# Kernel tuning notes

Measured on AMD Instinct MI355X. Metric: run time of the kernel, lower is better.

Reference implementation:

```python
import jax, jax.numpy as jnp
import numpy as np

I, H, B, T = 512, 512, 64, 1024


def _xavier(key, shape):
    fan_in, fan_out = shape
    lim = float(np.sqrt(6.0 / (fan_in + fan_out)))
    return jax.random.uniform(key, shape, jnp.float32, -lim, lim)


def setup_inputs() -> dict:
    key = jax.random.key(0)
    ks = jax.random.split(key, 9)
    inp = {"x": jax.random.normal(ks[0], (B, T, I), jnp.float32)}
    names = ["W_ii", "W_hi", "W_if", "W_hf", "W_ig", "W_hg", "W_io", "W_ho"]
    for n, k in zip(names, ks[1:]):
        shape = (I, H) if n[2] == "i" else (H, H)
        inp[n] = _xavier(k, shape)
    for n in ["b_ii", "b_hi", "b_if", "b_hf", "b_ig", "b_hg", "b_io", "b_ho"]:
        inp[n] = jnp.zeros((H,), jnp.float32)
    return inp


def _lstm(x, W_ii, b_ii, W_hi, b_hi, W_if, b_if, W_hf, b_hf,
          W_ig, b_ig, W_hg, b_hg, W_io, b_io, W_ho, b_ho):
    Bx, Tx = x.shape[0], x.shape[1]
    Hh = W_hi.shape[0]
    # Fuse the 4 input-side gate GEMMs into one: (B,T,I) @ (I,4H)
    Wx = jnp.concatenate([W_if, W_ii, W_ig, W_io], axis=1)          # (I,4H)
    bx = jnp.concatenate([b_if + b_hf, b_ii + b_hi, b_ig + b_hg, b_io + b_ho])
    Wh = jnp.concatenate([W_hf, W_hi, W_hg, W_ho], axis=1)          # (H,4H)
    x_proj = jnp.einsum("bti,ig->btg", x, Wx) + bx                  # (B,T,4H)

    def step(carry, xp_t):
        h, c = carry
        g = xp_t + h @ Wh                                           # (B,4H)
        f = jax.nn.sigmoid(g[:, 0 * Hh:1 * Hh])
        i = jax.nn.sigmoid(g[:, 1 * Hh:2 * Hh])
        gg = jnp.tanh(g[:, 2 * Hh:3 * Hh])
        o = jax.nn.sigmoid(g[:, 3 * Hh:4 * Hh])
        c = f * c + i * gg
        h = o * jnp.tanh(c)
        return (h, c), None

    h0 = jnp.zeros((Bx, Hh), x.dtype)
    c0 = jnp.zeros((Bx, Hh), x.dtype)
    (h, c), _ = jax.lax.scan(step, (h0, c0), jnp.swapaxes(x_proj, 0, 1))
    return h, c


def reference(x, W_ii, W_hi, W_if, W_hf, W_ig, W_hg, W_io, W_ho,
              b_ii, b_hi, b_if, b_hf, b_ig, b_hg, b_io, b_ho):
    return _lstm(x, W_ii, b_ii, W_hi, b_hi, W_if, b_if, W_hf, b_hf,
                 W_ig, b_ig, W_hg, b_hg, W_io, b_io, W_ho, b_ho)
```

## Files before the change

kernel.cpp:

```cpp
#include <hip/hip_runtime.h>
#include <hip/hip_bf16.h>
#include <stdint.h>

typedef __attribute__((ext_vector_type(8))) short short8;
typedef __attribute__((ext_vector_type(4))) float f32x4;
typedef __attribute__((ext_vector_type(4))) unsigned int u32x4;
typedef __attribute__((ext_vector_type(2))) unsigned int u32x2;

__device__ __forceinline__ unsigned short f2bf(float x) {
  unsigned int u = __builtin_bit_cast(unsigned int, x);
  u += 0x7FFFu + ((u >> 16) & 1u);
  return (unsigned short)(u >> 16);
}
__device__ __forceinline__ float bf2f(unsigned short u) {
  unsigned int v = ((unsigned int)u) << 16;
  return __builtin_bit_cast(float, v);
}
__device__ __forceinline__ unsigned int pk2(float a, float b) {
  return (unsigned int)f2bf(a) | ((unsigned int)f2bf(b) << 16);
}
__device__ __forceinline__ float sigm(float x) {
  return __builtin_amdgcn_rcpf(1.0f + __builtin_amdgcn_exp2f(-1.44269504f * x));
}
__device__ __forceinline__ float tanh_(float x) {
  return 2.0f * __builtin_amdgcn_rcpf(1.0f + __builtin_amdgcn_exp2f(-2.88539008f * x)) - 1.0f;
}
__device__ __forceinline__ f32x4 mfma16(short8 a, short8 b, f32x4 c) {
  return __builtin_amdgcn_mfma_f32_16x16x32_bf16(a, b, c, 0, 0, 0);
}
__device__ __forceinline__ short8 bc(u32x4 v) { return __builtin_bit_cast(short8, v); }

__global__ void lstm_prep(
    const float* __restrict__ Wif, const float* __restrict__ Wii,
    const float* __restrict__ Wig, const float* __restrict__ Wio,
    const float* __restrict__ Whf, const float* __restrict__ Whi,
    const float* __restrict__ Whg, const float* __restrict__ Who,
    const float* __restrict__ bif, const float* __restrict__ bhf,
    const float* __restrict__ bii, const float* __restrict__ bhi,
    const float* __restrict__ big, const float* __restrict__ bhg,
    const float* __restrict__ bio, const float* __restrict__ bho,
    unsigned short* __restrict__ WxT, unsigned short* __restrict__ WhT,
    float* __restrict__ bias, unsigned short* __restrict__ hring)
{
  const long NWX = 2048L * 512, NWH = 32L * 64 * 512;
  const long NR = 4L * 4 * 16 * 512;
  long total = NWX + NWH + 2048 + NR;
  for (long i = (long)blockIdx.x * blockDim.x + threadIdx.x; i < total;
       i += (long)gridDim.x * blockDim.x) {
    if (i < NWX) {
      int n = (int)(i >> 9), k = (int)(i & 511);
      int g = n >> 9, hc = n & 511;
      const float* W = (g == 0) ? Wif : (g == 1) ? Wii : (g == 2) ? Wig : Wio;
      WxT[i] = f2bf(W[k * 512 + hc]);
    } else if (i < NWX + NWH) {
      long r = i - NWX;
      int wg = (int)(r >> 15); int rest = (int)(r & 32767);
      int j = rest >> 9, k = rest & 511;
      int g = j >> 4, hc = wg * 16 + (j & 15);
      const float* W = (g == 0) ? Whf : (g == 1) ? Whi : (g == 2) ? Whg : Who;
      WhT[r] = f2bf(W[k * 512 + hc]);
    } else if (i < NWX + NWH + 2048) {
      int n = (int)(i - NWX - NWH);
      int g = n >> 9, hc = n & 511;
      const float* bi = (g == 0) ? bif : (g == 1) ? bii : (g == 2) ? big : bio;
      const float* bh = (g == 0) ? bhf : (g == 1) ? bhi : (g == 2) ? bhg : bho;
      bias[n] = bi[hc] + bh[hc];
    } else {
      long r = i - NWX - NWH - 2048;
      long rr = r & 32767;
      hring[r] = (rr < 8192) ? (unsigned short)0 : (unsigned short)0x8000u;
    }
  }
}

#define GP 56

__global__ __launch_bounds__(256) void lstm_xproj(
    const float* __restrict__ x, const unsigned short* __restrict__ WxT,
    const float* __restrict__ bias, unsigned short* __restrict__ xp)
{
  __shared__ unsigned short As[128 * GP];
  __shared__ unsigned short Bs[128 * GP];
  int bid = blockIdx.x;
  int mt = bid & 511, nt = bid >> 9;
  int m0 = mt << 7, n0 = nt << 7;
  int tid = threadIdx.x, lane = tid & 63, w = tid >> 6;
  int wm = w >> 1, wn = w & 1;
  int l15 = lane & 15, hi4 = lane >> 4;

  f32x4 acc[4][4] = {};
  int srow = tid >> 1, skq = (tid & 1) << 4;
  const float* xa = x + (size_t)(m0 + srow) * 512 + skq;
  const unsigned short* bsrc = WxT + (size_t)(n0 + srow) * 512 + skq;
  unsigned short* adst = As + srow * GP + skq;
  unsigned short* bdst = Bs + srow * GP + skq;

  for (int kt = 0; kt < 16; ++kt) {
    f32x4 a0 = *(const f32x4*)(xa + kt * 32);
    f32x4 a1 = *(const f32x4*)(xa + kt * 32 + 4);
    f32x4 a2 = *(const f32x4*)(xa + kt * 32 + 8);
    f32x4 a3 = *(const f32x4*)(xa + kt * 32 + 12);
    u32x4 wv0 = *(const u32x4*)(bsrc + kt * 32);
    u32x4 wv1 = *(const u32x4*)(bsrc + kt * 32 + 8);
    u32x4 p0, p1;
    p0[0] = pk2(a0[0], a0[1]); p0[1] = pk2(a0[2], a0[3]);
    p0[2] = pk2(a1[0], a1[1]); p0[3] = pk2(a1[2], a1[3]);
    p1[0] = pk2(a2[0], a2[1]); p1[1] = pk2(a2[2], a2[3]);
    p1[2] = pk2(a3[0], a3[1]); p1[3] = pk2(a3[2], a3[3]);
    *(u32x4*)adst = p0;  *(u32x4*)(adst + 8) = p1;
    *(u32x4*)bdst = wv0; *(u32x4*)(bdst + 8) = wv1;
    __syncthreads();
    short8 af[4], bfr[4];
    #pragma unroll
    for (int mb = 0; mb < 4; ++mb)
      af[mb] = *(const short8*)(As + (wm * 64 + mb * 16 + l15) * GP + hi4 * 8);
    #pragma unroll
    for (int nb = 0; nb < 4; ++nb)
      bfr[nb] = *(const short8*)(Bs + (wn * 64 + nb * 16 + l15) * GP + hi4 * 8);
    #pragma unroll
    for (int mb = 0; mb < 4; ++mb)
      #pragma unroll
      for (int nb = 0; nb < 4; ++nb)
        acc[mb][nb] = mfma16(af[mb], bfr[nb], acc[mb][nb]);
    __syncthreads();
  }
  #pragma unroll
  for (int nb = 0; nb < 4; ++nb) {
    int n = n0 + wn * 64 + nb * 16 + l15;
    int gate = n >> 9, hc = n & 511, wgc = hc >> 4, lcol = hc & 15;
    float bv = bias[n];
    #pragma unroll
    for (int mb = 0; mb < 4; ++mb) {
      int mbase = m0 + wm * 64 + mb * 16 + hi4 * 4;
      #pragma unroll
      for (int i = 0; i < 4; ++i) {
        int m = mbase + i;
        int tt = m & 1023, bb = m >> 10;
        int ddc = bb >> 4, rloc = bb & 15;
        int chi = rloc >> 2, cii = rloc & 3;
        size_t dst = ((((size_t)tt * 128 + ddc * 32 + wgc) * 4 + gate) * 64 +
                      (size_t)(chi * 16 + lcol)) * 4 + cii;
        xp[dst] = f2bf(acc[mb][nb][i] + bv);
      }
    }
  }
}

#define AWAIT(N) do { \
  asm volatile("s_waitcnt vmcnt(" #N ")" ::: "memory"); \
  __builtin_amdgcn_sched_barrier(0); } while (0)

#define PLD1(dst, vof, sb) \
  asm volatile("global_load_dwordx4 %0, %1, %2 sc0 sc1" \
               : "=v"(dst) : "v"(vof), "s"(sb))

#define XLD2(dst, a64) \
  asm volatile("global_load_dwordx2 %0, %1, off" : "=v"(dst) : "v"(a64))

__global__ __launch_bounds__(256, 1) void lstm_rec(
    const unsigned short* __restrict__ xp, const unsigned short* __restrict__ WhT,
    unsigned short* __restrict__ hring, float* __restrict__ out)
{
  __shared__ unsigned short hA[8192];
  __shared__ float pre[4][16][17];

  int wgG = blockIdx.x;
  int dd = wgG >> 5, wgl = wgG & 31;
  int tid = threadIdx.x, lane = tid & 63, g = tid >> 6;
  int l15 = lane & 15, hi4 = lane >> 4;

  short8 bw[16];
  {
    const unsigned short* wsrc =
        WhT + ((size_t)wgl * 64 + g * 16 + l15) * 512 + hi4 * 8;
    #pragma unroll
    for (int kk = 0; kk < 16; ++kk)
      bw[kk] = *(const short8*)(wsrc + kk * 32);
  }

  unsigned int voff[4], lbyt[4];
  #pragma unroll
  for (int k = 0; k < 4; ++k) {
    int gid = k * 256 + tid;
    int byt = gid * 16;
    int row = gid >> 6;
    voff[k] = (unsigned)byt;
    lbyt[k] = (unsigned)(byt ^ ((row & 7) << 4));
  }
  int gcol = tid & 63;
  unsigned own = (gcol == wgl * 2 || gcol == wgl * 2 + 1) ? 0xFu : 0x0u;

  const int r = (tid & 127) >> 3;
  const int cq = (tid & 7) * 2;
  float cst[2] = {0.f, 0.f};
  unsigned int vpub = (unsigned)(r * 1024 + (wgl * 16 + cq) * 2);
  unsigned int lown = (unsigned)((r * 1024 + (wgl * 16 + cq) * 2)
                                 ^ ((r & 7) << 4));

  unsigned long long xaddr = (unsigned long long)(uintptr_t)(
      xp + ((size_t)(wgG * 4 + g) * 64 + lane) * 4);

  u32x2 pc, pn;
  XLD2(pc, xaddr);

  const size_t dbase = (size_t)dd * 32768;

  u32x4 gb[4];
  {
    const unsigned short* hb = hring + dbase;
    #pragma unroll
    for (int k = 0; k < 4; ++k) PLD1(gb[k], voff[k], hb);
  }

  for (int t = 0; t < 1024; ++t) {
    const unsigned short* hb = hring + dbase + ((size_t)(t & 3) << 13);
    if (t >= 2 && tid < 128) {
      const unsigned short* hp = hring + dbase + ((size_t)((t - 2) & 3) << 13);
      unsigned int pv = 0x80008000u;
      asm volatile("global_store_dword %0, %1, %2 sc0 sc1"
                   :: "v"(vpub), "v"(pv), "s"(hp) : "memory");
    }
    {
      unsigned m = (t == 0) ? 0xFu : (0xFu & ~own);
      int spins = 0;
      for (;;) {
        AWAIT(0);
        unsigned nm = 0;
        #pragma unroll
        for (int k = 0; k < 4; ++k) {
          if ((m >> k) & 1u) {
            u32x4 v = gb[k];
            bool clean = (v[0] != 0x80008000u) && (v[1] != 0x80008000u) &&
                         (v[2] != 0x80008000u) && (v[3] != 0x80008000u);
            if (clean)
              *(u32x4*)((char*)hA + lbyt[k]) = v;
            else
              nm |= (1u << k);
          }
        }
        m = nm;
        if (m == 0u) break;
        if (++spins > (1 << 15)) break;
        #pragma unroll
        for (int k = 0; k < 4; ++k)
          if ((m >> k) & 1u) PLD1(gb[k], voff[k], hb);
      }
    }
    __syncthreads();

    f32x4 acc;
    #pragma unroll
    for (int i = 0; i < 4; ++i) {
      unsigned int dw = pc[i >> 1];
      unsigned short us = (i & 1) ? (unsigned short)(dw >> 16)
                                  : (unsigned short)(dw & 0xFFFFu);
      acc[i] = bf2f(us);
    }
    if (t < 1023) xaddr += 262144ULL;
    XLD2(pn, xaddr);

    #pragma unroll
    for (int kk = 0; kk < 16; ++kk) {
      int b0 = (l15 * 1024 + kk * 64 + hi4 * 16) ^ ((l15 & 7) << 4);
      short8 a0 = *(const short8*)((const char*)hA + b0);
      acc = mfma16(a0, bw[kk], acc);
    }
    #pragma unroll
    for (int i = 0; i < 4; ++i)
      pre[g][hi4 * 4 + i][l15] = acc[i];
    __syncthreads();

    if (t < 1023) {
      const unsigned short* hbn =
          hring + dbase + ((size_t)((t + 1) & 3) << 13);
      #pragma unroll
      for (int k = 0; k < 4; ++k)
        if (!((own >> k) & 1u)) PLD1(gb[k], voff[k], hbn);
    }

    if (tid < 128) {
      float hv[2];
      #pragma unroll
      for (int i = 0; i < 2; ++i) {
        float fg = sigm(pre[0][r][cq + i]);
        float ig = sigm(pre[1][r][cq + i]);
        float gg = tanh_(pre[2][r][cq + i]);
        float og = sigm(pre[3][r][cq + i]);
        float c = fg * cst[i] + ig * gg;
        cst[i] = c;
        hv[i] = og * tanh_(c);
      }
      if (t < 1023) {
        unsigned int u0 = f2bf(hv[0]), u1 = f2bf(hv[1]);
        if (u0 == 0x8000u) u0 = 0;
        if (u1 == 0x8000u) u1 = 0;
        unsigned int pk = u0 | (u1 << 16);
        const unsigned short* hbn =
            hring + dbase + ((size_t)((t + 1) & 3) << 13);
        asm volatile("global_store_dword %0, %1, %2 sc0 sc1"
                     :: "v"(vpub), "v"(pk), "s"(hbn) : "memory");
        *(unsigned int*)((char*)hA + lown) = pk;
      } else {
        int b = dd * 16 + r, col = wgl * 16 + cq;
        out[(size_t)b * 512 + col] = hv[0];
        out[(size_t)b * 512 + col + 1] = hv[1];
        out[32768 + (size_t)b * 512 + col] = cst[0];
        out[32768 + (size_t)b * 512 + col + 1] = cst[1];
      }
    }
    pc = pn;
  }
}

extern "C" void kernel_launch(void* const* d_in, const int* in_sizes, int n_in,
                              void* d_out, int out_size, void* d_ws, size_t ws_size,
                              hipStream_t stream) {
  const float* x   = (const float*)d_in[0];
  const float* Wii = (const float*)d_in[1];
  const float* Whi = (const float*)d_in[2];
  const float* Wif = (const float*)d_in[3];
  const float* Whf = (const float*)d_in[4];
  const float* Wig = (const float*)d_in[5];
  const float* Whg = (const float*)d_in[6];
  const float* Wio = (const float*)d_in[7];
  const float* Who = (const float*)d_in[8];
  const float* bii = (const float*)d_in[9];
  const float* bhi = (const float*)d_in[10];
  const float* bif = (const float*)d_in[11];
  const float* bhf = (const float*)d_in[12];
  const float* big = (const float*)d_in[13];
  const float* bhg = (const float*)d_in[14];
  const float* bio = (const float*)d_in[15];
  const float* bho = (const float*)d_in[16];

  char* ws = (char*)d_ws;
  size_t off = 0;
  auto alloc = [&](size_t bytes) {
    size_t p = off; off = (off + bytes + 255) & ~(size_t)255; return p;
  };
  unsigned short* WxT  = (unsigned short*)(ws + alloc(2048UL * 512 * 2));
  unsigned short* WhT  = (unsigned short*)(ws + alloc(32UL * 64 * 512 * 2));
  float*          bias = (float*)        (ws + alloc(2048UL * 4));
  unsigned short* hring= (unsigned short*)(ws + alloc(4UL * 4 * 16 * 512 * 2));
  unsigned short* xpb  = (unsigned short*)(ws + alloc(1024UL * 64 * 2048 * 2));
  if (off > ws_size) return;

  lstm_prep<<<2048, 256, 0, stream>>>(Wif, Wii, Wig, Wio, Whf, Whi, Whg, Who,
                                      bif, bhf, bii, bhi, big, bhg, bio, bho,
                                      WxT, WhT, bias, hring);
  lstm_xproj<<<8192, 256, 0, stream>>>(x, WxT, bias, xpb);
  lstm_rec<<<128, 256, 0, stream>>>(xpb, WhT, hring, (float*)d_out);
}
```

Measured before the change: 2.653 ms.

## Fuse input projection into recurrent kernel, overlapping it with the h-exchange wait

Removes the separate xproj GEMM kernel and its large bf16 intermediate buffer. Each recurrent workgroup now keeps its slice of Wx in registers and computes the x-projection for each timestep with MFMAs inside the time loop, starting from the bias. That work runs while the workgroup waits for the other workgroups to publish h. The cost is 16 more short8 registers per thread and redundant fp32 x loads from global memory on the serial critical path, since each of the 4 waves in a workgroup reads the same x rows.

```diff
diff --git a/kernel.cpp b/kernel.cpp
--- a/kernel.cpp
+++ b/kernel.cpp
@@ -5,16 +5,11 @@
 typedef __attribute__((ext_vector_type(8))) short short8;
 typedef __attribute__((ext_vector_type(4))) float f32x4;
 typedef __attribute__((ext_vector_type(4))) unsigned int u32x4;
-typedef __attribute__((ext_vector_type(2))) unsigned int u32x2;
 
 __device__ __forceinline__ unsigned short f2bf(float x) {
   unsigned int u = __builtin_bit_cast(unsigned int, x);
   u += 0x7FFFu + ((u >> 16) & 1u);
   return (unsigned short)(u >> 16);
-}
-__device__ __forceinline__ float bf2f(unsigned short u) {
-  unsigned int v = ((unsigned int)u) << 16;
-  return __builtin_bit_cast(float, v);
 }
 __device__ __forceinline__ unsigned int pk2(float a, float b) {
   return (unsigned int)f2bf(a) | ((unsigned int)f2bf(b) << 16);
@@ -73,79 +68,6 @@
   }
 }
 
-#define GP 56
-
-__global__ __launch_bounds__(256) void lstm_xproj(
-    const float* __restrict__ x, const unsigned short* __restrict__ WxT,
-    const float* __restrict__ bias, unsigned short* __restrict__ xp)
-{
-  __shared__ unsigned short As[128 * GP];
-  __shared__ unsigned short Bs[128 * GP];
-  int bid = blockIdx.x;
-  int mt = bid & 511, nt = bid >> 9;
-  int m0 = mt << 7, n0 = nt << 7;
-  int tid = threadIdx.x, lane = tid & 63, w = tid >> 6;
-  int wm = w >> 1, wn = w & 1;
-  int l15 = lane & 15, hi4 = lane >> 4;
-
-  f32x4 acc[4][4] = {};
-  int srow = tid >> 1, skq = (tid & 1) << 4;
-  const float* xa = x + (size_t)(m0 + srow) * 512 + skq;
-  const unsigned short* bsrc = WxT + (size_t)(n0 + srow) * 512 + skq;
-  unsigned short* adst = As + srow * GP + skq;
-  unsigned short* bdst = Bs + srow * GP + skq;
-
-  for (int kt = 0; kt < 16; ++kt) {
-    f32x4 a0 = *(const f32x4*)(xa + kt * 32);
-    f32x4 a1 = *(const f32x4*)(xa + kt * 32 + 4);
-    f32x4 a2 = *(const f32x4*)(xa + kt * 32 + 8);
-    f32x4 a3 = *(const f32x4*)(xa + kt * 32 + 12);
-    u32x4 wv0 = *(const u32x4*)(bsrc + kt * 32);
-    u32x4 wv1 = *(const u32x4*)(bsrc + kt * 32 + 8);
-    u32x4 p0, p1;
-    p0[0] = pk2(a0[0], a0[1]); p0[1] = pk2(a0[2], a0[3]);
-    p0[2] = pk2(a1[0], a1[1]); p0[3] = pk2(a1[2], a1[3]);
-    p1[0] = pk2(a2[0], a2[1]); p1[1] = pk2(a2[2], a2[3]);
-    p1[2] = pk2(a3[0], a3[1]); p1[3] = pk2(a3[2], a3[3]);
-    *(u32x4*)adst = p0;  *(u32x4*)(adst + 8) = p1;
-    *(u32x4*)bdst = wv0; *(u32x4*)(bdst + 8) = wv1;
-    __syncthreads();
-    short8 af[4], bfr[4];
-    #pragma unroll
-    for (int mb = 0; mb < 4; ++mb)
-      af[mb] = *(const short8*)(As + (wm * 64 + mb * 16 + l15) * GP + hi4 * 8);
-    #pragma unroll
-    for (int nb = 0; nb < 4; ++nb)
-      bfr[nb] = *(const short8*)(Bs + (wn * 64 + nb * 16 + l15) * GP + hi4 * 8);
-    #pragma unroll
-    for (int mb = 0; mb < 4; ++mb)
-      #pragma unroll
-      for (int nb = 0; nb < 4; ++nb)
-        acc[mb][nb] = mfma16(af[mb], bfr[nb], acc[mb][nb]);
-    __syncthreads();
-  }
-  #pragma unroll
-  for (int nb = 0; nb < 4; ++nb) {
-    int n = n0 + wn * 64 + nb * 16 + l15;
-    int gate = n >> 9, hc = n & 511, wgc = hc >> 4, lcol = hc & 15;
-    float bv = bias[n];
-    #pragma unroll
-    for (int mb = 0; mb < 4; ++mb) {
-      int mbase = m0 + wm * 64 + mb * 16 + hi4 * 4;
-      #pragma unroll
-      for (int i = 0; i < 4; ++i) {
-        int m = mbase + i;
-        int tt = m & 1023, bb = m >> 10;
-        int ddc = bb >> 4, rloc = bb & 15;
-        int chi = rloc >> 2, cii = rloc & 3;
-        size_t dst = ((((size_t)tt * 128 + ddc * 32 + wgc) * 4 + gate) * 64 +
-                      (size_t)(chi * 16 + lcol)) * 4 + cii;
-        xp[dst] = f2bf(acc[mb][nb][i] + bv);
-      }
-    }
-  }
-}
-
 #define AWAIT(N) do { \
   asm volatile("s_waitcnt vmcnt(" #N ")" ::: "memory"); \
   __builtin_amdgcn_sched_barrier(0); } while (0)
@@ -154,11 +76,9 @@
   asm volatile("global_load_dwordx4 %0, %1, %2 sc0 sc1" \
                : "=v"(dst) : "v"(vof), "s"(sb))
 
-#define XLD2(dst, a64) \
-  asm volatile("global_load_dwordx2 %0, %1, off" : "=v"(dst) : "v"(a64))
-
 __global__ __launch_bounds__(256, 1) void lstm_rec(
-    const unsigned short* __restrict__ xp, const unsigned short* __restrict__ WhT,
+    const float* __restrict__ x, const unsigned short* __restrict__ WhT,
+    const unsigned short* __restrict__ WxT, const float* __restrict__ bias,
     unsigned short* __restrict__ hring, float* __restrict__ out)
 {
   __shared__ unsigned short hA[8192];
@@ -169,14 +89,19 @@
   int tid = threadIdx.x, lane = tid & 63, g = tid >> 6;
   int l15 = lane & 15, hi4 = lane >> 4;
 
-  short8 bw[16];
+  short8 bw[16], bwx[16];
   {
     const unsigned short* wsrc =
         WhT + ((size_t)wgl * 64 + g * 16 + l15) * 512 + hi4 * 8;
-    #pragma unroll
-    for (int kk = 0; kk < 16; ++kk)
+    const unsigned short* xsrc =
+        WxT + ((size_t)(g * 512 + wgl * 16 + l15)) * 512 + hi4 * 8;
+    #pragma unroll
+    for (int kk = 0; kk < 16; ++kk) {
       bw[kk] = *(const short8*)(wsrc + kk * 32);
-  }
+      bwx[kk] = *(const short8*)(xsrc + kk * 32);
+    }
+  }
+  const float bv = bias[g * 512 + wgl * 16 + l15];
 
   unsigned int voff[4], lbyt[4];
   #pragma unroll
@@ -197,11 +122,8 @@
   unsigned int lown = (unsigned)((r * 1024 + (wgl * 16 + cq) * 2)
                                  ^ ((r & 7) << 4));
 
-  unsigned long long xaddr = (unsigned long long)(uintptr_t)(
-      xp + ((size_t)(wgG * 4 + g) * 64 + lane) * 4);
-
-  u32x2 pc, pn;
-  XLD2(pc, xaddr);
+  const float* xrow =
+      x + ((size_t)(dd * 16 + l15) * 1024) * 512 + hi4 * 8;
 
   const size_t dbase = (size_t)dd * 32768;
 
@@ -220,10 +142,41 @@
       asm volatile("global_store_dword %0, %1, %2 sc0 sc1"
                    :: "v"(vpub), "v"(pv), "s"(hp) : "memory");
     }
+    unsigned m = (t == 0) ? 0xFu : (0xFu & ~own);
     {
-      unsigned m = (t == 0) ? 0xFu : (0xFu & ~own);
+      AWAIT(0);
+      unsigned nm = 0;
+      #pragma unroll
+      for (int k = 0; k < 4; ++k) {
+        if ((m >> k) & 1u) {
+          u32x4 v = gb[k];
+          bool clean = (v[0] != 0x80008000u) && (v[1] != 0x80008000u) &&
+                       (v[2] != 0x80008000u) && (v[3] != 0x80008000u);
+          if (clean)
+            *(u32x4*)((char*)hA + lbyt[k]) = v;
+          else
+            nm |= (1u << k);
+        }
+      }
+      m = nm;
+      #pragma unroll
+      for (int k = 0; k < 4; ++k)
+        if ((m >> k) & 1u) PLD1(gb[k], voff[k], hb);
+    }
+    f32x4 acc = {bv, bv, bv, bv};
+    #pragma unroll
+    for (int kk = 0; kk < 16; ++kk) {
+      f32x4 lo = *(const f32x4*)(xrow + kk * 32);
+      f32x4 hi = *(const f32x4*)(xrow + kk * 32 + 4);
+      u32x4 p;
+      p[0] = pk2(lo[0], lo[1]); p[1] = pk2(lo[2], lo[3]);
+      p[2] = pk2(hi[0], hi[1]); p[3] = pk2(hi[2], hi[3]);
+      acc = mfma16(bc(p), bwx[kk], acc);
+    }
+    xrow += 512;
+    {
       int spins = 0;
-      for (;;) {
+      while (m != 0u) {
         AWAIT(0);
         unsigned nm = 0;
         #pragma unroll
@@ -248,17 +201,6 @@
     }
     __syncthreads();
 
-    f32x4 acc;
-    #pragma unroll
-    for (int i = 0; i < 4; ++i) {
-      unsigned int dw = pc[i >> 1];
-      unsigned short us = (i & 1) ? (unsigned short)(dw >> 16)
-                                  : (unsigned short)(dw & 0xFFFFu);
-      acc[i] = bf2f(us);
-    }
-    if (t < 1023) xaddr += 262144ULL;
-    XLD2(pn, xaddr);
-
     #pragma unroll
     for (int kk = 0; kk < 16; ++kk) {
       int b0 = (l15 * 1024 + kk * 64 + hi4 * 16) ^ ((l15 & 7) << 4);
@@ -308,7 +250,6 @@
         out[32768 + (size_t)b * 512 + col + 1] = cst[1];
       }
     }
-    pc = pn;
   }
 }
 
@@ -342,12 +283,10 @@
   unsigned short* WhT  = (unsigned short*)(ws + alloc(32UL * 64 * 512 * 2));
   float*          bias = (float*)        (ws + alloc(2048UL * 4));
   unsigned short* hring= (unsigned short*)(ws + alloc(4UL * 4 * 16 * 512 * 2));
-  unsigned short* xpb  = (unsigned short*)(ws + alloc(1024UL * 64 * 2048 * 2));
   if (off > ws_size) return;
 
   lstm_prep<<<2048, 256, 0, stream>>>(Wif, Wii, Wig, Wio, Whf, Whi, Whg, Who,
                                       bif, bhf, bii, bhi, big, bhg, bio, bho,
                                       WxT, WhT, bias, hring);
-  lstm_xproj<<<8192, 256, 0, stream>>>(x, WxT, bias, xpb);
-  lstm_rec<<<128, 256, 0, stream>>>(xpb, WhT, hring, (float*)d_out);
-}
+  lstm_rec<<<128, 256, 0, stream>>>(x, WhT, WxT, bias, hring, (float*)d_out);
+}
```

New measurement: 8.097 ms. 205% more time.

## Fuse input projection GEMM and recurrence into one kernel with chunk counters

Applied to the files above, without the earlier changes.

Merges the x-projection GEMM and the recurrent LSTM kernel into a single launch. The first 128 blocks run the recurrence while the remaining blocks compute x_proj tiles, ordered by time chunk. Each producer tile bumps a per-(batch-group, 128-timestep chunk) counter, and the recurrent blocks spin on that counter before consuming each chunk. The goal is to overlap the large GEMM with the serial recurrence and drop a kernel boundary. In exchange it relies on the 128 recurrent blocks being resident first and adds spin-waits and coherent (sc0 sc1) stores and loads.

```diff
diff --git a/kernel.cpp b/kernel.cpp
--- a/kernel.cpp
+++ b/kernel.cpp
@@ -40,11 +40,12 @@
     const float* __restrict__ big, const float* __restrict__ bhg,
     const float* __restrict__ bio, const float* __restrict__ bho,
     unsigned short* __restrict__ WxT, unsigned short* __restrict__ WhT,
-    float* __restrict__ bias, unsigned short* __restrict__ hring)
+    float* __restrict__ bias, unsigned short* __restrict__ hring,
+    int* __restrict__ cnt)
 {
   const long NWX = 2048L * 512, NWH = 32L * 64 * 512;
   const long NR = 4L * 4 * 16 * 512;
-  long total = NWX + NWH + 2048 + NR;
+  long total = NWX + NWH + 2048 + NR + 32;
   for (long i = (long)blockIdx.x * blockDim.x + threadIdx.x; i < total;
        i += (long)gridDim.x * blockDim.x) {
     if (i < NWX) {
@@ -65,83 +66,12 @@
       const float* bi = (g == 0) ? bif : (g == 1) ? bii : (g == 2) ? big : bio;
       const float* bh = (g == 0) ? bhf : (g == 1) ? bhi : (g == 2) ? bhg : bho;
       bias[n] = bi[hc] + bh[hc];
-    } else {
+    } else if (i < NWX + NWH + 2048 + NR) {
       long r = i - NWX - NWH - 2048;
       long rr = r & 32767;
       hring[r] = (rr < 8192) ? (unsigned short)0 : (unsigned short)0x8000u;
-    }
-  }
-}
-
-#define GP 56
-
-__global__ __launch_bounds__(256) void lstm_xproj(
-    const float* __restrict__ x, const unsigned short* __restrict__ WxT,
-    const float* __restrict__ bias, unsigned short* __restrict__ xp)
-{
-  __shared__ unsigned short As[128 * GP];
-  __shared__ unsigned short Bs[128 * GP];
-  int bid = blockIdx.x;
-  int mt = bid & 511, nt = bid >> 9;
-  int m0 = mt << 7, n0 = nt << 7;
-  int tid = threadIdx.x, lane = tid & 63, w = tid >> 6;
-  int wm = w >> 1, wn = w & 1;
-  int l15 = lane & 15, hi4 = lane >> 4;
-
-  f32x4 acc[4][4] = {};
-  int srow = tid >> 1, skq = (tid & 1) << 4;
-  const float* xa = x + (size_t)(m0 + srow) * 512 + skq;
-  const unsigned short* bsrc = WxT + (size_t)(n0 + srow) * 512 + skq;
-  unsigned short* adst = As + srow * GP + skq;
-  unsigned short* bdst = Bs + srow * GP + skq;
-
-  for (int kt = 0; kt < 16; ++kt) {
-    f32x4 a0 = *(const f32x4*)(xa + kt * 32);
-    f32x4 a1 = *(const f32x4*)(xa + kt * 32 + 4);
-    f32x4 a2 = *(const f32x4*)(xa + kt * 32 + 8);
-    f32x4 a3 = *(const f32x4*)(xa + kt * 32 + 12);
-    u32x4 wv0 = *(const u32x4*)(bsrc + kt * 32);
-    u32x4 wv1 = *(const u32x4*)(bsrc + kt * 32 + 8);
-    u32x4 p0, p1;
-    p0[0] = pk2(a0[0], a0[1]); p0[1] = pk2(a0[2], a0[3]);
-    p0[2] = pk2(a1[0], a1[1]); p0[3] = pk2(a1[2], a1[3]);
-    p1[0] = pk2(a2[0], a2[1]); p1[1] = pk2(a2[2], a2[3]);
-    p1[2] = pk2(a3[0], a3[1]); p1[3] = pk2(a3[2], a3[3]);
-    *(u32x4*)adst = p0;  *(u32x4*)(adst + 8) = p1;
-    *(u32x4*)bdst = wv0; *(u32x4*)(bdst + 8) = wv1;
-    __syncthreads();
-    short8 af[4], bfr[4];
-    #pragma unroll
-    for (int mb = 0; mb < 4; ++mb)
-      af[mb] = *(const short8*)(As + (wm * 64 + mb * 16 + l15) * GP + hi4 * 8);
-    #pragma unroll
-    for (int nb = 0; nb < 4; ++nb)
-      bfr[nb] = *(const short8*)(Bs + (wn * 64 + nb * 16 + l15) * GP + hi4 * 8);
-    #pragma unroll
-    for (int mb = 0; mb < 4; ++mb)
-      #pragma unroll
-      for (int nb = 0; nb < 4; ++nb)
-        acc[mb][nb] = mfma16(af[mb], bfr[nb], acc[mb][nb]);
-    __syncthreads();
-  }
-  #pragma unroll
-  for (int nb = 0; nb < 4; ++nb) {
-    int n = n0 + wn * 64 + nb * 16 + l15;
-    int gate = n >> 9, hc = n & 511, wgc = hc >> 4, lcol = hc & 15;
-    float bv = bias[n];
-    #pragma unroll
-    for (int mb = 0; mb < 4; ++mb) {
-      int mbase = m0 + wm * 64 + mb * 16 + hi4 * 4;
-      #pragma unroll
-      for (int i = 0; i < 4; ++i) {
-        int m = mbase + i;
-        int tt = m & 1023, bb = m >> 10;
-        int ddc = bb >> 4, rloc = bb & 15;
-        int chi = rloc >> 2, cii = rloc & 3;
-        size_t dst = ((((size_t)tt * 128 + ddc * 32 + wgc) * 4 + gate) * 64 +
-                      (size_t)(chi * 16 + lcol)) * 4 + cii;
-        xp[dst] = f2bf(acc[mb][nb][i] + bv);
-      }
+    } else {
+      cnt[i - NWX - NWH - 2048 - NR] = 0;
     }
   }
 }
@@ -155,18 +85,106 @@
                : "=v"(dst) : "v"(vof), "s"(sb))
 
 #define XLD2(dst, a64) \
-  asm volatile("global_load_dwordx2 %0, %1, off" : "=v"(dst) : "v"(a64))
-
-__global__ __launch_bounds__(256, 1) void lstm_rec(
-    const unsigned short* __restrict__ xp, const unsigned short* __restrict__ WhT,
-    unsigned short* __restrict__ hring, float* __restrict__ out)
+  asm volatile("global_load_dwordx2 %0, %1, off sc0 sc1" \
+               : "=v"(dst) : "v"(a64))
+
+#define GP 56
+
+__global__ __launch_bounds__(256, 1) void lstm_fused(
+    const float* __restrict__ x, const unsigned short* __restrict__ WxT,
+    const unsigned short* __restrict__ WhT, const float* __restrict__ bias,
+    unsigned short* __restrict__ hring, unsigned short* __restrict__ xp,
+    int* __restrict__ cnt, float* __restrict__ out)
 {
-  __shared__ unsigned short hA[8192];
-  __shared__ float pre[4][16][17];
-
-  int wgG = blockIdx.x;
+  __shared__ __align__(16) unsigned char smem[28672];
+  int bid = blockIdx.x;
+  int tid = threadIdx.x, lane = tid & 63;
+
+  if (bid >= 128) {
+    unsigned short* As = (unsigned short*)smem;
+    unsigned short* Bs = As + 128 * GP;
+    int id = bid - 128;
+    int c = id >> 10, rem = id & 1023;
+    int bb = rem >> 4, nt = rem & 15;
+    int mt = bb * 8 + c;
+    int m0 = mt << 7, n0 = nt << 7;
+    int w = tid >> 6;
+    int wm = w >> 1, wn = w & 1;
+    int l15 = lane & 15, hi4 = lane >> 4;
+
+    f32x4 acc[4][4] = {};
+    int srow = tid >> 1, skq = (tid & 1) << 4;
+    const float* xa = x + (size_t)(m0 + srow) * 512 + skq;
+    const unsigned short* bsrc = WxT + (size_t)(n0 + srow) * 512 + skq;
+    unsigned short* adst = As + srow * GP + skq;
+    unsigned short* bdst = Bs + srow * GP + skq;
+
+    for (int kt = 0; kt < 16; ++kt) {
+      f32x4 a0 = *(const f32x4*)(xa + kt * 32);
+      f32x4 a1 = *(const f32x4*)(xa + kt * 32 + 4);
+      f32x4 a2 = *(const f32x4*)(xa + kt * 32 + 8);
+      f32x4 a3 = *(const f32x4*)(xa + kt * 32 + 12);
+      u32x4 wv0 = *(const u32x4*)(bsrc + kt * 32);
+      u32x4 wv1 = *(const u32x4*)(bsrc + kt * 32 + 8);
+      u32x4 p0, p1;
+      p0[0] = pk2(a0[0], a0[1]); p0[1] = pk2(a0[2], a0[3]);
+      p0[2] = pk2(a1[0], a1[1]); p0[3] = pk2(a1[2], a1[3]);
+      p1[0] = pk2(a2[0], a2[1]); p1[1] = pk2(a2[2], a2[3]);
+      p1[2] = pk2(a3[0], a3[1]); p1[3] = pk2(a3[2], a3[3]);
+      *(u32x4*)adst = p0;  *(u32x4*)(adst + 8) = p1;
+      *(u32x4*)bdst = wv0; *(u32x4*)(bdst + 8) = wv1;
+      __syncthreads();
+      short8 af[4], bfr[4];
+      #pragma unroll
+      for (int mb = 0; mb < 4; ++mb)
+        af[mb] = *(const short8*)(As + (wm * 64 + mb * 16 + l15) * GP + hi4 * 8);
+      #pragma unroll
+      for (int nb = 0; nb < 4; ++nb)
+        bfr[nb] = *(const short8*)(Bs + (wn * 64 + nb * 16 + l15) * GP + hi4 * 8);
+      #pragma unroll
+      for (int mb = 0; mb < 4; ++mb)
+        #pragma unroll
+        for (int nb = 0; nb < 4; ++nb)
+          acc[mb][nb] = mfma16(af[mb], bfr[nb], acc[mb][nb]);
+      __syncthreads();
+    }
+    #pragma unroll
+    for (int nb = 0; nb < 4; ++nb) {
+      int n = n0 + wn * 64 + nb * 16 + l15;
+      int gate = n >> 9, hc = n & 511, wgc = hc >> 4, lcol = hc & 15;
+      float bv = bias[n];
+      #pragma unroll
+      for (int mb = 0; mb < 4; ++mb) {
+        int mbase = m0 + wm * 64 + mb * 16 + hi4 * 4;
+        #pragma unroll
+        for (int i = 0; i < 4; ++i) {
+          int m = mbase + i;
+          int tt = m & 1023, bbm = m >> 10;
+          int ddc = bbm >> 4, rloc = bbm & 15;
+          int chi = rloc >> 2, cii = rloc & 3;
+          size_t dst = ((((size_t)tt * 128 + ddc * 32 + wgc) * 4 + gate) * 64 +
+                        (size_t)(chi * 16 + lcol)) * 4 + cii;
+          unsigned long long a64 =
+              (unsigned long long)(uintptr_t)(xp + dst);
+          unsigned int val = (unsigned int)f2bf(acc[mb][nb][i] + bv);
+          asm volatile("global_store_short %0, %1, off sc0 sc1"
+                       :: "v"(a64), "v"(val) : "memory");
+        }
+      }
+    }
+    AWAIT(0);
+    __syncthreads();
+    if (tid == 0)
+      atomicAdd(&cnt[(bb >> 4) * 8 + c], 1);
+    return;
+  }
+
+  unsigned short* hA = (unsigned short*)smem;
+  float (*pre)[16][17] = (float (*)[16][17])(smem + 16384);
+
+  int wgG = bid;
   int dd = wgG >> 5, wgl = wgG & 31;
-  int tid = threadIdx.x, lane = tid & 63, g = tid >> 6;
+  int g = tid >> 6;
   int l15 = lane & 15, hi4 = lane >> 4;
 
   short8 bw[16];
@@ -200,9 +218,6 @@
   unsigned long long xaddr = (unsigned long long)(uintptr_t)(
       xp + ((size_t)(wgG * 4 + g) * 64 + lane) * 4);
 
-  u32x2 pc, pn;
-  XLD2(pc, xaddr);
-
   const size_t dbase = (size_t)dd * 32768;
 
   u32x4 gb[4];
@@ -211,6 +226,21 @@
     #pragma unroll
     for (int k = 0; k < 4; ++k) PLD1(gb[k], voff[k], hb);
   }
+
+  {
+    const int* ca = cnt + dd * 8;
+    int spins = 0;
+    for (;;) {
+      int cv;
+      asm volatile("global_load_dword %0, %1, %2 sc0 sc1"
+                   : "=v"(cv) : "v"((unsigned)0), "s"(ca));
+      AWAIT(0);
+      if (cv >= 256) break;
+      if (++spins > (1 << 18)) break;
+    }
+  }
+  u32x2 pc, pn;
+  XLD2(pc, xaddr);
 
   for (int t = 0; t < 1024; ++t) {
     const unsigned short* hb = hring + dbase + ((size_t)(t & 3) << 13);
@@ -256,7 +286,21 @@
                                   : (unsigned short)(dw & 0xFFFFu);
       acc[i] = bf2f(us);
     }
-    if (t < 1023) xaddr += 262144ULL;
+    if (t < 1023) {
+      xaddr += 262144ULL;
+      if (((t + 1) & 127) == 0) {
+        const int* ca = cnt + dd * 8 + ((t + 1) >> 7);
+        int spins = 0;
+        for (;;) {
+          int cv;
+          asm volatile("global_load_dword %0, %1, %2 sc0 sc1"
+                       : "=v"(cv) : "v"((unsigned)0), "s"(ca));
+          AWAIT(0);
+          if (cv >= 256) break;
+          if (++spins > (1 << 18)) break;
+        }
+      }
+    }
     XLD2(pn, xaddr);
 
     #pragma unroll
@@ -342,12 +386,13 @@
   unsigned short* WhT  = (unsigned short*)(ws + alloc(32UL * 64 * 512 * 2));
   float*          bias = (float*)        (ws + alloc(2048UL * 4));
   unsigned short* hring= (unsigned short*)(ws + alloc(4UL * 4 * 16 * 512 * 2));
+  int*            cnt  = (int*)          (ws + alloc(32UL * 4));
   unsigned short* xpb  = (unsigned short*)(ws + alloc(1024UL * 64 * 2048 * 2));
   if (off > ws_size) return;
 
   lstm_prep<<<2048, 256, 0, stream>>>(Wif, Wii, Wig, Wio, Whf, Whi, Whg, Who,
                                       bif, bhf, bii, bhi, big, bhg, bio, bho,
-                                      WxT, WhT, bias, hring);
-  lstm_xproj<<<8192, 256, 0, stream>>>(x, WxT, bias, xpb);
-  lstm_rec<<<128, 256, 0, stream>>>(xpb, WhT, hring, (float*)d_out);
-}
+                                      WxT, WhT, bias, hring, cnt);
+  lstm_fused<<<8320, 256, 0, stream>>>(x, WxT, WhT, bias, hring, xpb, cnt,
+                                       (float*)d_out);
+}
```

After: 2.847 ms. 7.3% more time.
